# Optimization experiments

Measured on AMD Instinct MI355X. Metric: run time of the kernel, lower is better.

## Reference

```python
import jax, jax.numpy as jnp
import numpy as np

N_NODES = 50000
N_EDGES = 800000

def _sage_conv(x, src, dst, W, b, n_nodes):
    # DGL SAGEConv aggregator_type='gcn':
    #   h_neigh = (sum_{u in N(v)} x_u + x_v) / (in_deg(v) + 1)
    #   out = h_neigh @ W.T + b   (fc_self unused for gcn aggregator)
    agg = jax.ops.segment_sum(x[src], dst, num_segments=n_nodes)  # [N, d]
    deg = jax.ops.segment_sum(jnp.ones((src.shape[0],), x.dtype), dst, num_segments=n_nodes)
    h = (agg + x) / (deg + 1.0)[:, None]
    return h @ W.T + b

def setup_inputs() -> dict:
    key = jax.random.key(0)
    ks = jax.random.split(key, 9)
    d_in, d_hid, d_out = 128, 128, 64
    x = jax.random.normal(ks[0], (N_NODES, d_in), dtype=jnp.float32)
    src = jax.random.randint(ks[1], (N_EDGES,), 0, N_NODES, dtype=jnp.int32)
    dst = jax.random.randint(ks[2], (N_EDGES,), 0, N_NODES, dtype=jnp.int32)
    def glorot(k, shape):
        fan = shape[0] + shape[1]
        return jax.random.normal(k, shape, dtype=jnp.float32) * jnp.sqrt(2.0 / fan)
    W1 = glorot(ks[3], (d_hid, d_in))
    b1 = jnp.zeros((d_hid,), jnp.float32)
    W2 = glorot(ks[4], (d_hid, d_hid))
    b2 = jnp.zeros((d_hid,), jnp.float32)
    W3 = glorot(ks[5], (d_out, d_hid))
    b3 = jnp.zeros((d_out,), jnp.float32)
    return {"x": x, "src": src, "dst": dst, "W1": W1, "b1": b1,
            "W2": W2, "b2": b2, "W3": W3, "b3": b3}

def reference(x, src, dst, W1, b1, W2, b2, W3, b3):
    n = x.shape[0]
    h = jax.nn.relu(_sage_conv(x, src, dst, W1, b1, n))
    h = jax.nn.relu(_sage_conv(h, src, dst, W2, b2, n))
    h = jax.nn.sigmoid(_sage_conv(h, src, dst, W3, b3, n))
    return h
```

## Files before the change

kernel.cpp:

```cpp
#include <hip/hip_runtime.h>
#include <hip/hip_bf16.h>
#include <math.h>


#define NFEAT 128
#define BSH   6
#define NBUKP 1024
#define EPB2  1024
#define CAP   1600

typedef __attribute__((ext_vector_type(8))) short bf16x8;
typedef __attribute__((ext_vector_type(4))) float f32x4;

__device__ __forceinline__ unsigned short f2bf(float f) {
    unsigned u = __float_as_uint(f);
    u += 0x7fffu + ((u >> 16) & 1u);
    return (unsigned short)(u >> 16);
}
__device__ __forceinline__ float bflo(unsigned u) { return __uint_as_float(u << 16); }
__device__ __forceinline__ float bfhi(unsigned u) { return __uint_as_float(u & 0xffff0000u); }


__global__ __launch_bounds__(256) void cvt_scatter_kernel(
        const int* __restrict__ src, const int* __restrict__ dst,
        int* __restrict__ cursor, unsigned long long* __restrict__ pairs,
        int E, int SBLK,
        const float* __restrict__ x,  const float* __restrict__ W1,
        const float* __restrict__ W2, const float* __restrict__ W3,
        ushort* __restrict__ xb, ushort* __restrict__ w1,
        ushort* __restrict__ w2, ushort* __restrict__ w3,
        int nx, int n1, int n2, int n3) {
    __shared__ int hist[NBUKP];
    __shared__ int sc[NBUKP];
    __shared__ int lcur[NBUKP];
    __shared__ int lbase[NBUKP];
    __shared__ unsigned long long stage[EPB2];
    __shared__ int destIdx[EPB2];
    __shared__ int nLocalSh;

    const int t = threadIdx.x;

    if (blockIdx.x >= SBLK) {
        int i = (blockIdx.x - SBLK) * 256 + t;
        const float* s; ushort* d; int off;
        if (i < nx)                      { s = x;  d = xb; off = i; }
        else if (i < nx + n1)            { s = W1; d = w1; off = i - nx; }
        else if (i < nx + n1 + n2)       { s = W2; d = w2; off = i - nx - n1; }
        else if (i < nx + n1 + n2 + n3)  { s = W3; d = w3; off = i - nx - n1 - n2; }
        else return;
        float4 f = *(const float4*)(s + (size_t)off * 4);
        *(ushort4*)(d + (size_t)off * 4) = make_ushort4(f2bf(f.x), f2bf(f.y), f2bf(f.z), f2bf(f.w));
        return;
    }

#pragma unroll
    for (int k = 0; k < NBUKP / 256; ++k) {
        hist[t + 256 * k] = 0;
        lcur[t + 256 * k] = 0;
    }
    __syncthreads();

    const int base = blockIdx.x * EPB2;
    int bb[EPB2 / 256];
    unsigned long long pr[EPB2 / 256];
#pragma unroll
    for (int j = 0; j < EPB2 / 256; ++j) {
        int e = base + t + 256 * j;
        bb[j] = -1;
        if (e < E) {
            int s = src[e], d = dst[e];
            int b = d >> BSH;
            bb[j] = b;
            pr[j] = ((unsigned long long)(unsigned)d << 32) | (unsigned)s;
            atomicAdd(&hist[b], 1);
        }
    }
    __syncthreads();
#pragma unroll
    for (int k = 0; k < NBUKP / 256; ++k) sc[t + 256 * k] = hist[t + 256 * k];
    __syncthreads();
    for (int off = 1; off < NBUKP; off <<= 1) {
        int v0 = (t >= off) ? sc[t - off] : 0;
        int v1 = (t + 256 >= off) ? sc[t + 256 - off] : 0;
        int v2 = (t + 512 >= off) ? sc[t + 512 - off] : 0;
        int v3 = (t + 768 >= off) ? sc[t + 768 - off] : 0;
        __syncthreads();
        sc[t] += v0; sc[t + 256] += v1; sc[t + 512] += v2; sc[t + 768] += v3;
        __syncthreads();
    }
    if (t == 255) nLocalSh = sc[NBUKP - 1];
#pragma unroll
    for (int k = 0; k < NBUKP / 256; ++k) sc[t + 256 * k] -= hist[t + 256 * k];
    for (int b = t; b < NBUKP; b += 256) {
        int h = hist[b];
        if (h > 0) lbase[b] = atomicAdd(&cursor[b], h);
    }
    __syncthreads();
#pragma unroll
    for (int j = 0; j < EPB2 / 256; ++j) {
        int b = bb[j];
        if (b >= 0) {
            int slot = atomicAdd(&lcur[b], 1);
            int spos = sc[b] + slot;
            stage[spos] = pr[j];
            int rel = lbase[b] + slot;
            destIdx[spos] = (rel < CAP) ? (b * CAP + rel) : -1;
        }
    }
    __syncthreads();
    const int nLocal = nLocalSh;
#pragma unroll
    for (int j = 0; j < EPB2 / 256; ++j) {
        int i = t + 256 * j;
        if (i < nLocal && destIdx[i] >= 0) pairs[destIdx[i]] = stage[i];
    }
}


__global__ __launch_bounds__(512) void build_csr(const unsigned long long* __restrict__ pairs,
                                                 const int* __restrict__ cursor,
                                                 int* __restrict__ row_beg,
                                                 int* __restrict__ row_end,
                                                 float* __restrict__ deg_inv,
                                                 int* __restrict__ col_idx, int N) {
    __shared__ unsigned long long pairsL[CAP];
    __shared__ int srcS[CAP];
    __shared__ int nhist[64];
    __shared__ int npref[64];
    __shared__ int ncur[64];

    const int t = threadIdx.x;
    const int b = blockIdx.x;
    const int nodeBase = b << BSH;
    const int eBeg = b * CAP;
    int eCnt = cursor[b];
    if (eCnt > CAP) eCnt = CAP;

    if (t < 64) { nhist[t] = 0; ncur[t] = 0; }
    __syncthreads();

    for (int i = t; i < eCnt; i += 512) {
        unsigned long long p = pairs[eBeg + i];
        pairsL[i] = p;
        atomicAdd(&nhist[(int)(p >> 32) - nodeBase], 1);
    }
    __syncthreads();
    if (t < 64) npref[t] = nhist[t];
    __syncthreads();
    for (int off = 1; off < 64; off <<= 1) {
        int v = (t < 64 && t >= off) ? npref[t - off] : 0;
        __syncthreads();
        if (t < 64) npref[t] += v;
        __syncthreads();
    }
    if (t < 64) npref[t] -= nhist[t];
    if (t < 64 && nodeBase + t < N) {
        row_beg[nodeBase + t] = eBeg + npref[t];
        row_end[nodeBase + t] = eBeg + npref[t] + nhist[t];
        deg_inv[nodeBase + t] = 1.0f / (float)(nhist[t] + 1);
    }
    __syncthreads();
    for (int i = t; i < eCnt; i += 512) {
        unsigned long long p = pairsL[i];
        int d = (int)(p >> 32) - nodeBase;
        int slot = atomicAdd(&ncur[d], 1);
        srcS[npref[d] + slot] = (int)(unsigned)p;
    }
    __syncthreads();
    for (int i = t; i < eCnt; i += 512) col_idx[eBeg + i] = srcS[i];
}


#define ACC8(u)                                                     \
    a0 += bflo((u).x); a1 += bfhi((u).x);                           \
    a2 += bflo((u).y); a3 += bfhi((u).y);                           \
    a4 += bflo((u).z); a5 += bfhi((u).z);                           \
    a6 += bflo((u).w); a7 += bfhi((u).w);

template<int SECOND>
__global__ __launch_bounds__(256) void fused_agg_gemm_kernel(
        const ushort* __restrict__ Xb,
        const int* __restrict__ row_beg,
        const int* __restrict__ row_end,
        const float* __restrict__ deg_inv,
        const ushort* __restrict__ Wb,
        const float* __restrict__ bias,
        const ushort* __restrict__ W3b,
        const int* __restrict__ col_idx,
        ushort* __restrict__ outB, int N) {
    __shared__ ushort A[16][136];
    __shared__ ushort H2[SECOND ? 16 : 1][136];

    const int t    = threadIdx.x;
    const int w    = t >> 6;
    const int lane = t & 63;
    const int g    = lane >> 4;
    const int f    = lane & 15;
    const int base = blockIdx.x * 16;
    const uint4* X4 = (const uint4*)Xb;

    {
        const int v = base + w * 4 + g;
        const int beg = (v < N) ? row_beg[v] : 0;
        const int end = (v < N) ? row_end[v] : 0;
        const int deg = end - beg;

        uint4 us = (v < N) ? X4[(size_t)v * 16 + f] : make_uint4(0, 0, 0, 0);
        float inv = (v < N) ? deg_inv[v] : 0.f;

        int c0 = 0, c1 = 0;
        if (f < deg)      c0 = col_idx[beg + f];
        if (f + 16 < deg) c1 = col_idx[beg + 16 + f];

        float a0 = 0.f, a1 = 0.f, a2 = 0.f, a3 = 0.f;
        float a4 = 0.f, a5 = 0.f, a6 = 0.f, a7 = 0.f;

        const int nf = deg < 32 ? deg : 32;
        int j = 0;
        for (; j + 7 < nf; j += 8) {
            const int cc = (j & 16) ? c1 : c0;
            int s0 = __shfl(cc, (j & 15) + 0, 16);
            int s1 = __shfl(cc, (j & 15) + 1, 16);
            int s2 = __shfl(cc, (j & 15) + 2, 16);
            int s3 = __shfl(cc, (j & 15) + 3, 16);
            int s4 = __shfl(cc, (j & 15) + 4, 16);
            int s5 = __shfl(cc, (j & 15) + 5, 16);
            int s6 = __shfl(cc, (j & 15) + 6, 16);
            int s7 = __shfl(cc, (j & 15) + 7, 16);
            uint4 u0 = X4[(size_t)s0 * 16 + f];
            uint4 u1 = X4[(size_t)s1 * 16 + f];
            uint4 u2 = X4[(size_t)s2 * 16 + f];
            uint4 u3 = X4[(size_t)s3 * 16 + f];
            uint4 u4 = X4[(size_t)s4 * 16 + f];
            uint4 u5 = X4[(size_t)s5 * 16 + f];
            uint4 u6 = X4[(size_t)s6 * 16 + f];
            uint4 u7 = X4[(size_t)s7 * 16 + f];
            ACC8(u0); ACC8(u1); ACC8(u2); ACC8(u3);
            ACC8(u4); ACC8(u5); ACC8(u6); ACC8(u7);
        }
        for (; j < nf; ++j) {
            const int cc = (j & 16) ? c1 : c0;
            int s0 = __shfl(cc, j & 15, 16);
            uint4 u = X4[(size_t)s0 * 16 + f];
            ACC8(u);
        }
        for (int e = beg + 32; e < end; ++e) {
            uint4 u = X4[(size_t)col_idx[e] * 16 + f];
            ACC8(u);
        }

        if (v < N) {
            uint4 r;
            r.x = (unsigned)f2bf((a0 + bflo(us.x)) * inv) | ((unsigned)f2bf((a1 + bfhi(us.x)) * inv) << 16);
            r.y = (unsigned)f2bf((a2 + bflo(us.y)) * inv) | ((unsigned)f2bf((a3 + bfhi(us.y)) * inv) << 16);
            r.z = (unsigned)f2bf((a4 + bflo(us.z)) * inv) | ((unsigned)f2bf((a5 + bfhi(us.z)) * inv) << 16);
            r.w = (unsigned)f2bf((a6 + bflo(us.w)) * inv) | ((unsigned)f2bf((a7 + bfhi(us.w)) * inv) << 16);
            ((uint4*)&A[w * 4 + g][0])[f] = r;
        }
    }
    __syncthreads();

    const int m    = lane & 15;
    const int quad = lane >> 4;
    f32x4 acc0 = {0.f, 0.f, 0.f, 0.f};
    f32x4 acc1 = {0.f, 0.f, 0.f, 0.f};
    {
        const ushort* arow = &A[m][quad * 8];
        const ushort* wrow = Wb + (size_t)(w * 32 + m) * NFEAT + quad * 8;
#pragma unroll
        for (int k0 = 0; k0 < NFEAT; k0 += 32) {
            bf16x8 a  = *(const bf16x8*)(arow + k0);
            bf16x8 bA = *(const bf16x8*)(wrow + k0);
            bf16x8 bB = *(const bf16x8*)(wrow + 16 * NFEAT + k0);
            acc0 = __builtin_amdgcn_mfma_f32_16x16x32_bf16(a, bA, acc0, 0, 0, 0);
            acc1 = __builtin_amdgcn_mfma_f32_16x16x32_bf16(a, bB, acc1, 0, 0, 0);
        }
    }
    const float bv0 = bias[w * 32 + m];
    const float bv1 = bias[w * 32 + 16 + m];

    if (!SECOND) {
#pragma unroll
        for (int r = 0; r < 4; ++r) {
            int row = base + quad * 4 + r;
            if (row < N) {
                outB[(size_t)row * NFEAT + w * 32 + m]      = f2bf(fmaxf(acc0[r] + bv0, 0.f));
                outB[(size_t)row * NFEAT + w * 32 + 16 + m] = f2bf(fmaxf(acc1[r] + bv1, 0.f));
            }
        }
    } else {
#pragma unroll
        for (int r = 0; r < 4; ++r) {
            H2[quad * 4 + r][w * 32 + m]      = f2bf(fmaxf(acc0[r] + bv0, 0.f));
            H2[quad * 4 + r][w * 32 + 16 + m] = f2bf(fmaxf(acc1[r] + bv1, 0.f));
        }
        __syncthreads();
        f32x4 acc3 = {0.f, 0.f, 0.f, 0.f};
        const ushort* hrow  = &H2[m][quad * 8];
        const ushort* w3row = W3b + (size_t)(w * 16 + m) * NFEAT + quad * 8;
#pragma unroll
        for (int k0 = 0; k0 < NFEAT; k0 += 32) {
            bf16x8 a = *(const bf16x8*)(hrow + k0);
            bf16x8 b = *(const bf16x8*)(w3row + k0);
            acc3 = __builtin_amdgcn_mfma_f32_16x16x32_bf16(a, b, acc3, 0, 0, 0);
        }
#pragma unroll
        for (int r = 0; r < 4; ++r) {
            int row = base + quad * 4 + r;
            if (row < N) outB[(size_t)row * 64 + w * 16 + m] = f2bf(acc3[r]);
        }
    }
}


__global__ __launch_bounds__(256) void agg64_sigmoid_kernel(const ushort* __restrict__ Gb,
                                                            const int* __restrict__ row_beg,
                                                            const int* __restrict__ row_end,
                                                            const float* __restrict__ deg_inv,
                                                            const int* __restrict__ col_idx,
                                                            const float* __restrict__ bias,
                                                            float* __restrict__ out, int N) {
    const int wp   = blockIdx.x * (blockDim.x >> 6) + (threadIdx.x >> 6);
    const int lane = threadIdx.x & 63;
    const int half = lane >> 5;
    const int hl   = lane & 31;
    const int v    = wp * 2 + half;
    const bool act = (v < N);

    int beg = 0, end = 0;
    if (act) { beg = row_beg[v]; end = row_end[v]; }
    const int deg = end - beg;
    const unsigned* Gu = (const unsigned*)Gb;

    int cidx = 0;
    if (hl < deg) cidx = col_idx[beg + hl];

    float a0 = 0.f, a1 = 0.f, b0 = 0.f, b1 = 0.f;
    float c0 = 0.f, c1 = 0.f, d0 = 0.f, d1 = 0.f;
    const int nfast = deg < 32 ? deg : 32;
    int j = 0;
    for (; j + 7 < nfast; j += 8) {
        int s0 = __shfl(cidx, j + 0, 32);
        int s1 = __shfl(cidx, j + 1, 32);
        int s2 = __shfl(cidx, j + 2, 32);
        int s3 = __shfl(cidx, j + 3, 32);
        int s4 = __shfl(cidx, j + 4, 32);
        int s5 = __shfl(cidx, j + 5, 32);
        int s6 = __shfl(cidx, j + 6, 32);
        int s7 = __shfl(cidx, j + 7, 32);
        unsigned u0 = Gu[(size_t)s0 * 32 + hl];
        unsigned u1 = Gu[(size_t)s1 * 32 + hl];
        unsigned u2 = Gu[(size_t)s2 * 32 + hl];
        unsigned u3 = Gu[(size_t)s3 * 32 + hl];
        unsigned u4 = Gu[(size_t)s4 * 32 + hl];
        unsigned u5 = Gu[(size_t)s5 * 32 + hl];
        unsigned u6 = Gu[(size_t)s6 * 32 + hl];
        unsigned u7 = Gu[(size_t)s7 * 32 + hl];
        a0 += bflo(u0); a1 += bfhi(u0);
        b0 += bflo(u1); b1 += bfhi(u1);
        c0 += bflo(u2); c1 += bfhi(u2);
        d0 += bflo(u3); d1 += bfhi(u3);
        a0 += bflo(u4); a1 += bfhi(u4);
        b0 += bflo(u5); b1 += bfhi(u5);
        c0 += bflo(u6); c1 += bfhi(u6);
        d0 += bflo(u7); d1 += bfhi(u7);
    }
    for (; j + 3 < nfast; j += 4) {
        int s0 = __shfl(cidx, j + 0, 32);
        int s1 = __shfl(cidx, j + 1, 32);
        int s2 = __shfl(cidx, j + 2, 32);
        int s3 = __shfl(cidx, j + 3, 32);
        unsigned u0 = Gu[(size_t)s0 * 32 + hl];
        unsigned u1 = Gu[(size_t)s1 * 32 + hl];
        unsigned u2 = Gu[(size_t)s2 * 32 + hl];
        unsigned u3 = Gu[(size_t)s3 * 32 + hl];
        a0 += bflo(u0); a1 += bfhi(u0);
        b0 += bflo(u1); b1 += bfhi(u1);
        c0 += bflo(u2); c1 += bfhi(u2);
        d0 += bflo(u3); d1 += bfhi(u3);
    }
    for (; j < nfast; ++j) {
        int s0 = __shfl(cidx, j, 32);
        unsigned u0 = Gu[(size_t)s0 * 32 + hl];
        a0 += bflo(u0); a1 += bfhi(u0);
    }
    for (int e = beg + 32; e < end; ++e) {
        unsigned u0 = Gu[(size_t)col_idx[e] * 32 + hl];
        a0 += bflo(u0); a1 += bfhi(u0);
    }
    if (act) {
        unsigned us = Gu[(size_t)v * 32 + hl];
        float inv = deg_inv[v];
        float r0 = (a0 + b0 + c0 + d0 + bflo(us)) * inv + bias[hl * 2 + 0];
        float r1 = (a1 + b1 + c1 + d1 + bfhi(us)) * inv + bias[hl * 2 + 1];
        r0 = 1.0f / (1.0f + __expf(-r0));
        r1 = 1.0f / (1.0f + __expf(-r1));
        *(float2*)(out + (size_t)v * 64 + hl * 2) = make_float2(r0, r1);
    }
}


static inline size_t align256(size_t x) { return (x + 255) & ~(size_t)255; }

extern "C" void kernel_launch(void* const* d_in, const int* in_sizes, int n_in,
                              void* d_out, int out_size, void* d_ws, size_t ws_size,
                              hipStream_t stream) {
    const float* x   = (const float*)d_in[0];
    const int*   src = (const int*)d_in[1];
    const int*   dst = (const int*)d_in[2];
    const float* W1  = (const float*)d_in[3];
    const float* b1  = (const float*)d_in[4];
    const float* W2  = (const float*)d_in[5];
    const float* b2  = (const float*)d_in[6];
    const float* W3  = (const float*)d_in[7];
    const float* b3  = (const float*)d_in[8];
    float*       out = (float*)d_out;

    const int N = in_sizes[0] / NFEAT;
    const int E = in_sizes[1];
    const int D_OUT = in_sizes[7] / NFEAT;
    const int NBUK = (N + (1 << BSH) - 1) >> BSH;
    const int SBLK = (E + EPB2 - 1) / EPB2;

    char* ws = (char*)d_ws;
    int* row_beg      = (int*)ws;  ws += align256((size_t)N * 4);
    int* row_end      = (int*)ws;  ws += align256((size_t)N * 4);
    float* deg_inv    = (float*)ws; ws += align256((size_t)N * 4);
    int* cursor       = (int*)ws;  ws += align256((size_t)NBUKP * 4);
    int* col_idx      = (int*)ws;  ws += align256((size_t)NBUK * CAP * 4);
    ushort* w1bf      = (ushort*)ws; ws += align256((size_t)NFEAT * NFEAT * 2);
    ushort* w2bf      = (ushort*)ws; ws += align256((size_t)NFEAT * NFEAT * 2);
    ushort* w3bf      = (ushort*)ws; ws += align256((size_t)D_OUT * NFEAT * 2);
    ushort* xbf       = (ushort*)ws; ws += align256((size_t)N * NFEAT * 2);
    ushort* h1bf      = (ushort*)ws; ws += align256((size_t)N * NFEAT * 2);
    ushort* gbf = xbf;
    unsigned long long* pairs = (unsigned long long*)h1bf;

    const int nx = N * NFEAT / 4;
    const int n1 = NFEAT * NFEAT / 4, n2 = NFEAT * NFEAT / 4, n3 = D_OUT * NFEAT / 4;
    const int CVTB = (nx + n1 + n2 + n3 + 255) / 256;

    hipMemsetAsync(cursor, 0, (size_t)NBUKP * 4, stream);
    cvt_scatter_kernel<<<SBLK + CVTB, 256, 0, stream>>>(
        src, dst, cursor, pairs, E, SBLK,
        x, W1, W2, W3, xbf, w1bf, w2bf, w3bf, nx, n1, n2, n3);

    build_csr<<<NBUK, 512, 0, stream>>>(pairs, cursor, row_beg, row_end, deg_inv, col_idx, N);

    const int fusedBlocks = (N + 15) / 16;
    const int agg64Blocks = (N + 7) / 8;

    fused_agg_gemm_kernel<0><<<fusedBlocks, 256, 0, stream>>>(
        xbf, row_beg, row_end, deg_inv, w1bf, b1, nullptr, col_idx, h1bf, N);
    fused_agg_gemm_kernel<1><<<fusedBlocks, 256, 0, stream>>>(
        h1bf, row_beg, row_end, deg_inv, w2bf, b2, w3bf, col_idx, gbf, N);
    agg64_sigmoid_kernel<<<agg64Blocks, 256, 0, stream>>>(
        gbf, row_beg, row_end, deg_inv, col_idx, b3, out, N);
}
```

Measured before the change: 233.4 us.

## Merge all stages into one cooperative persistent kernel with grid syncs

Replaces the memset plus five separate kernel launches with a single cooperative kernel that runs the convert, scatter, CSR build, two fused aggregate-GEMM layers and the final aggregation as phases separated by grid-wide barriers. Blocks loop over virtual block indices, and shared memory is a single reused byte buffer. The aim is to remove launch overhead and inter-kernel gaps. In exchange, occupancy is capped at the cooperative grid size, the convert phase no longer overlaps the scatter phase, build_csr drops from 512 to 256 threads, and every phase boundary adds a grid sync.

```diff
diff --git a/kernel.cpp b/kernel.cpp
--- a/kernel.cpp
+++ b/kernel.cpp
@@ -1,6 +1,9 @@
 #include <hip/hip_runtime.h>
+#include <hip/hip_cooperative_groups.h>
 #include <hip/hip_bf16.h>
 #include <math.h>
+
+namespace cg = cooperative_groups;
 
 
 #define NFEAT 128
@@ -8,9 +11,23 @@
 #define NBUKP 1024
 #define EPB2  1024
 #define CAP   1600
-
+#define SMEM_BYTES 28680
+
+typedef unsigned long long ull;
 typedef __attribute__((ext_vector_type(8))) short bf16x8;
 typedef __attribute__((ext_vector_type(4))) float f32x4;
+
+struct MegaArgs {
+    const int* src; const int* dst;
+    int* cursor; ull* pairs;
+    const float* x; const float* W1; const float* W2; const float* W3;
+    const float* b1; const float* b2; const float* b3;
+    ushort* xb; ushort* w1b; ushort* w2b; ushort* w3b;
+    int* row_beg; int* row_end; float* deg_inv; int* col_idx;
+    ushort* h1; ushort* g; float* out;
+    int E, N, SBLK, NBUK, fusedB, agg64B;
+    int nx, n1, n2, n3, cvt_total;
+};
 
 __device__ __forceinline__ unsigned short f2bf(float f) {
     unsigned u = __float_as_uint(f);
@@ -21,57 +38,45 @@
 __device__ __forceinline__ float bfhi(unsigned u) { return __uint_as_float(u & 0xffff0000u); }
 
 
-__global__ __launch_bounds__(256) void cvt_scatter_kernel(
-        const int* __restrict__ src, const int* __restrict__ dst,
-        int* __restrict__ cursor, unsigned long long* __restrict__ pairs,
-        int E, int SBLK,
-        const float* __restrict__ x,  const float* __restrict__ W1,
-        const float* __restrict__ W2, const float* __restrict__ W3,
-        ushort* __restrict__ xb, ushort* __restrict__ w1,
-        ushort* __restrict__ w2, ushort* __restrict__ w3,
-        int nx, int n1, int n2, int n3) {
-    __shared__ int hist[NBUKP];
-    __shared__ int sc[NBUKP];
-    __shared__ int lcur[NBUKP];
-    __shared__ int lbase[NBUKP];
-    __shared__ unsigned long long stage[EPB2];
-    __shared__ int destIdx[EPB2];
-    __shared__ int nLocalSh;
-
-    const int t = threadIdx.x;
-
-    if (blockIdx.x >= SBLK) {
-        int i = (blockIdx.x - SBLK) * 256 + t;
+__device__ void phase_cvt(const MegaArgs& a, int gtid, int gsz) {
+    for (int i = gtid; i < a.cvt_total; i += gsz) {
         const float* s; ushort* d; int off;
-        if (i < nx)                      { s = x;  d = xb; off = i; }
-        else if (i < nx + n1)            { s = W1; d = w1; off = i - nx; }
-        else if (i < nx + n1 + n2)       { s = W2; d = w2; off = i - nx - n1; }
-        else if (i < nx + n1 + n2 + n3)  { s = W3; d = w3; off = i - nx - n1 - n2; }
-        else return;
+        if (i < a.nx)                              { s = a.x;  d = a.xb;  off = i; }
+        else if (i < a.nx + a.n1)                  { s = a.W1; d = a.w1b; off = i - a.nx; }
+        else if (i < a.nx + a.n1 + a.n2)           { s = a.W2; d = a.w2b; off = i - a.nx - a.n1; }
+        else                                       { s = a.W3; d = a.w3b; off = i - a.nx - a.n1 - a.n2; }
         float4 f = *(const float4*)(s + (size_t)off * 4);
         *(ushort4*)(d + (size_t)off * 4) = make_ushort4(f2bf(f.x), f2bf(f.y), f2bf(f.z), f2bf(f.w));
-        return;
-    }
-
-#pragma unroll
-    for (int k = 0; k < NBUKP / 256; ++k) {
-        hist[t + 256 * k] = 0;
-        lcur[t + 256 * k] = 0;
-    }
-    __syncthreads();
-
-    const int base = blockIdx.x * EPB2;
+    }
+    for (int i = gtid; i < NBUKP; i += gsz) a.cursor[i] = 0;
+}
+
+
+__device__ void phase_scatter(const MegaArgs& a, int vb, int t, char* smem) {
+    ull* stage    = (ull*)smem;
+    int* hist     = (int*)(smem + 8192);
+    int* sc       = (int*)(smem + 12288);
+    int* lcur     = (int*)(smem + 16384);
+    int* lbase    = (int*)(smem + 20480);
+    int* destIdx  = (int*)(smem + 24576);
+    int* nLocalSh = (int*)(smem + 28672);
+
+#pragma unroll
+    for (int k = 0; k < NBUKP / 256; ++k) { hist[t + 256 * k] = 0; lcur[t + 256 * k] = 0; }
+    __syncthreads();
+
+    const int base = vb * EPB2;
     int bb[EPB2 / 256];
-    unsigned long long pr[EPB2 / 256];
+    ull pr[EPB2 / 256];
 #pragma unroll
     for (int j = 0; j < EPB2 / 256; ++j) {
         int e = base + t + 256 * j;
         bb[j] = -1;
-        if (e < E) {
-            int s = src[e], d = dst[e];
+        if (e < a.E) {
+            int s = a.src[e], d = a.dst[e];
             int b = d >> BSH;
             bb[j] = b;
-            pr[j] = ((unsigned long long)(unsigned)d << 32) | (unsigned)s;
+            pr[j] = ((ull)(unsigned)d << 32) | (unsigned)s;
             atomicAdd(&hist[b], 1);
         }
     }
@@ -88,12 +93,12 @@
         sc[t] += v0; sc[t + 256] += v1; sc[t + 512] += v2; sc[t + 768] += v3;
         __syncthreads();
     }
-    if (t == 255) nLocalSh = sc[NBUKP - 1];
+    if (t == 255) *nLocalSh = sc[NBUKP - 1];
 #pragma unroll
     for (int k = 0; k < NBUKP / 256; ++k) sc[t + 256 * k] -= hist[t + 256 * k];
     for (int b = t; b < NBUKP; b += 256) {
         int h = hist[b];
-        if (h > 0) lbase[b] = atomicAdd(&cursor[b], h);
+        if (h > 0) lbase[b] = atomicAdd(&a.cursor[b], h);
     }
     __syncthreads();
 #pragma unroll
@@ -108,39 +113,33 @@
         }
     }
     __syncthreads();
-    const int nLocal = nLocalSh;
+    const int nLocal = *nLocalSh;
 #pragma unroll
     for (int j = 0; j < EPB2 / 256; ++j) {
         int i = t + 256 * j;
-        if (i < nLocal && destIdx[i] >= 0) pairs[destIdx[i]] = stage[i];
-    }
-}
-
-
-__global__ __launch_bounds__(512) void build_csr(const unsigned long long* __restrict__ pairs,
-                                                 const int* __restrict__ cursor,
-                                                 int* __restrict__ row_beg,
-                                                 int* __restrict__ row_end,
-                                                 float* __restrict__ deg_inv,
-                                                 int* __restrict__ col_idx, int N) {
-    __shared__ unsigned long long pairsL[CAP];
-    __shared__ int srcS[CAP];
-    __shared__ int nhist[64];
-    __shared__ int npref[64];
-    __shared__ int ncur[64];
-
-    const int t = threadIdx.x;
-    const int b = blockIdx.x;
-    const int nodeBase = b << BSH;
-    const int eBeg = b * CAP;
-    int eCnt = cursor[b];
+        if (i < nLocal && destIdx[i] >= 0) a.pairs[destIdx[i]] = stage[i];
+    }
+    __syncthreads();
+}
+
+
+__device__ void phase_csr(const MegaArgs& a, int vb, int t, char* smem) {
+    ull* pairsL = (ull*)smem;
+    int* srcS   = (int*)(smem + 12800);
+    int* nhist  = (int*)(smem + 19200);
+    int* npref  = (int*)(smem + 19456);
+    int* ncur   = (int*)(smem + 19712);
+
+    const int nodeBase = vb << BSH;
+    const int eBeg = vb * CAP;
+    int eCnt = a.cursor[vb];
     if (eCnt > CAP) eCnt = CAP;
 
     if (t < 64) { nhist[t] = 0; ncur[t] = 0; }
     __syncthreads();
 
-    for (int i = t; i < eCnt; i += 512) {
-        unsigned long long p = pairs[eBeg + i];
+    for (int i = t; i < eCnt; i += 256) {
+        ull p = a.pairs[eBeg + i];
         pairsL[i] = p;
         atomicAdd(&nhist[(int)(p >> 32) - nodeBase], 1);
     }
@@ -154,20 +153,21 @@
         __syncthreads();
     }
     if (t < 64) npref[t] -= nhist[t];
-    if (t < 64 && nodeBase + t < N) {
-        row_beg[nodeBase + t] = eBeg + npref[t];
-        row_end[nodeBase + t] = eBeg + npref[t] + nhist[t];
-        deg_inv[nodeBase + t] = 1.0f / (float)(nhist[t] + 1);
-    }
-    __syncthreads();
-    for (int i = t; i < eCnt; i += 512) {
-        unsigned long long p = pairsL[i];
+    if (t < 64 && nodeBase + t < a.N) {
+        a.row_beg[nodeBase + t] = eBeg + npref[t];
+        a.row_end[nodeBase + t] = eBeg + npref[t] + nhist[t];
+        a.deg_inv[nodeBase + t] = 1.0f / (float)(nhist[t] + 1);
+    }
+    __syncthreads();
+    for (int i = t; i < eCnt; i += 256) {
+        ull p = pairsL[i];
         int d = (int)(p >> 32) - nodeBase;
         int slot = atomicAdd(&ncur[d], 1);
         srcS[npref[d] + slot] = (int)(unsigned)p;
     }
     __syncthreads();
-    for (int i = t; i < eCnt; i += 512) col_idx[eBeg + i] = srcS[i];
+    for (int i = t; i < eCnt; i += 256) a.col_idx[eBeg + i] = srcS[i];
+    __syncthreads();
 }
 
 
@@ -178,35 +178,33 @@
     a6 += bflo((u).w); a7 += bfhi((u).w);
 
 template<int SECOND>
-__global__ __launch_bounds__(256) void fused_agg_gemm_kernel(
-        const ushort* __restrict__ Xb,
-        const int* __restrict__ row_beg,
-        const int* __restrict__ row_end,
-        const float* __restrict__ deg_inv,
-        const ushort* __restrict__ Wb,
-        const float* __restrict__ bias,
-        const ushort* __restrict__ W3b,
-        const int* __restrict__ col_idx,
-        ushort* __restrict__ outB, int N) {
-    __shared__ ushort A[16][136];
-    __shared__ ushort H2[SECOND ? 16 : 1][136];
-
-    const int t    = threadIdx.x;
+__device__ void phase_fused(const MegaArgs& a_, int vb, int t, char* smem) {
+    ushort (*A)[136]  = (ushort(*)[136])smem;
+    ushort (*H2)[136] = (ushort(*)[136])(smem + 4352);
+
+    const ushort* Xb   = SECOND ? a_.h1  : a_.xb;
+    const ushort* Wb   = SECOND ? a_.w2b : a_.w1b;
+    const float*  bias = SECOND ? a_.b2  : a_.b1;
+    const ushort* W3b  = a_.w3b;
+    ushort*       outB = SECOND ? a_.g   : a_.h1;
+    const int N = a_.N;
+    const int* __restrict__ col_idx = a_.col_idx;
+
     const int w    = t >> 6;
     const int lane = t & 63;
     const int g    = lane >> 4;
     const int f    = lane & 15;
-    const int base = blockIdx.x * 16;
+    const int base = vb * 16;
     const uint4* X4 = (const uint4*)Xb;
 
     {
         const int v = base + w * 4 + g;
-        const int beg = (v < N) ? row_beg[v] : 0;
-        const int end = (v < N) ? row_end[v] : 0;
+        const int beg = (v < N) ? a_.row_beg[v] : 0;
+        const int end = (v < N) ? a_.row_end[v] : 0;
         const int deg = end - beg;
 
         uint4 us = (v < N) ? X4[(size_t)v * 16 + f] : make_uint4(0, 0, 0, 0);
-        float inv = (v < N) ? deg_inv[v] : 0.f;
+        float inv = (v < N) ? a_.deg_inv[v] : 0.f;
 
         int c0 = 0, c1 = 0;
         if (f < deg)      c0 = col_idx[beg + f];
@@ -269,11 +267,11 @@
         const ushort* wrow = Wb + (size_t)(w * 32 + m) * NFEAT + quad * 8;
 #pragma unroll
         for (int k0 = 0; k0 < NFEAT; k0 += 32) {
-            bf16x8 a  = *(const bf16x8*)(arow + k0);
+            bf16x8 av = *(const bf16x8*)(arow + k0);
             bf16x8 bA = *(const bf16x8*)(wrow + k0);
             bf16x8 bB = *(const bf16x8*)(wrow + 16 * NFEAT + k0);
-            acc0 = __builtin_amdgcn_mfma_f32_16x16x32_bf16(a, bA, acc0, 0, 0, 0);
-            acc1 = __builtin_amdgcn_mfma_f32_16x16x32_bf16(a, bB, acc1, 0, 0, 0);
+            acc0 = __builtin_amdgcn_mfma_f32_16x16x32_bf16(av, bA, acc0, 0, 0, 0);
+            acc1 = __builtin_amdgcn_mfma_f32_16x16x32_bf16(av, bB, acc1, 0, 0, 0);
         }
     }
     const float bv0 = bias[w * 32 + m];
@@ -300,9 +298,9 @@
         const ushort* w3row = W3b + (size_t)(w * 16 + m) * NFEAT + quad * 8;
 #pragma unroll
         for (int k0 = 0; k0 < NFEAT; k0 += 32) {
-            bf16x8 a = *(const bf16x8*)(hrow + k0);
-            bf16x8 b = *(const bf16x8*)(w3row + k0);
-            acc3 = __builtin_amdgcn_mfma_f32_16x16x32_bf16(a, b, acc3, 0, 0, 0);
+            bf16x8 av = *(const bf16x8*)(hrow + k0);
+            bf16x8 bv = *(const bf16x8*)(w3row + k0);
+            acc3 = __builtin_amdgcn_mfma_f32_16x16x32_bf16(av, bv, acc3, 0, 0, 0);
         }
 #pragma unroll
         for (int r = 0; r < 4; ++r) {
@@ -310,30 +308,25 @@
             if (row < N) outB[(size_t)row * 64 + w * 16 + m] = f2bf(acc3[r]);
         }
     }
-}
-
-
-__global__ __launch_bounds__(256) void agg64_sigmoid_kernel(const ushort* __restrict__ Gb,
-                                                            const int* __restrict__ row_beg,
-                                                            const int* __restrict__ row_end,
-                                                            const float* __restrict__ deg_inv,
-                                                            const int* __restrict__ col_idx,
-                                                            const float* __restrict__ bias,
-                                                            float* __restrict__ out, int N) {
-    const int wp   = blockIdx.x * (blockDim.x >> 6) + (threadIdx.x >> 6);
-    const int lane = threadIdx.x & 63;
+    __syncthreads();
+}
+
+
+__device__ void phase_agg64(const MegaArgs& a, int vb, int t) {
+    const int wp   = vb * 4 + (t >> 6);
+    const int lane = t & 63;
     const int half = lane >> 5;
     const int hl   = lane & 31;
     const int v    = wp * 2 + half;
-    const bool act = (v < N);
+    const bool act = (v < a.N);
 
     int beg = 0, end = 0;
-    if (act) { beg = row_beg[v]; end = row_end[v]; }
+    if (act) { beg = a.row_beg[v]; end = a.row_end[v]; }
     const int deg = end - beg;
-    const unsigned* Gu = (const unsigned*)Gb;
+    const unsigned* Gu = (const unsigned*)a.g;
 
     int cidx = 0;
-    if (hl < deg) cidx = col_idx[beg + hl];
+    if (hl < deg) cidx = a.col_idx[beg + hl];
 
     float a0 = 0.f, a1 = 0.f, b0 = 0.f, b1 = 0.f;
     float c0 = 0.f, c1 = 0.f, d0 = 0.f, d1 = 0.f;
@@ -385,18 +378,63 @@
         a0 += bflo(u0); a1 += bfhi(u0);
     }
     for (int e = beg + 32; e < end; ++e) {
-        unsigned u0 = Gu[(size_t)col_idx[e] * 32 + hl];
+        unsigned u0 = Gu[(size_t)a.col_idx[e] * 32 + hl];
         a0 += bflo(u0); a1 += bfhi(u0);
     }
     if (act) {
         unsigned us = Gu[(size_t)v * 32 + hl];
-        float inv = deg_inv[v];
-        float r0 = (a0 + b0 + c0 + d0 + bflo(us)) * inv + bias[hl * 2 + 0];
-        float r1 = (a1 + b1 + c1 + d1 + bfhi(us)) * inv + bias[hl * 2 + 1];
+        float inv = a.deg_inv[v];
+        float r0 = (a0 + b0 + c0 + d0 + bflo(us)) * inv + a.b3[hl * 2 + 0];
+        float r1 = (a1 + b1 + c1 + d1 + bfhi(us)) * inv + a.b3[hl * 2 + 1];
         r0 = 1.0f / (1.0f + __expf(-r0));
         r1 = 1.0f / (1.0f + __expf(-r1));
-        *(float2*)(out + (size_t)v * 64 + hl * 2) = make_float2(r0, r1);
-    }
+        *(float2*)(a.out + (size_t)v * 64 + hl * 2) = make_float2(r0, r1);
+    }
+}
+
+
+__global__ __launch_bounds__(256) void mega_kernel(MegaArgs a) {
+    __shared__ __align__(16) char smem[SMEM_BYTES];
+    cg::grid_group grid = cg::this_grid();
+    const int t = threadIdx.x;
+    const int gtid = blockIdx.x * 256 + t;
+    const int gsz  = gridDim.x * 256;
+
+    phase_cvt(a, gtid, gsz);
+    __threadfence(); grid.sync();
+    for (int vb = blockIdx.x; vb < a.SBLK; vb += gridDim.x) phase_scatter(a, vb, t, smem);
+    __threadfence(); grid.sync();
+    for (int vb = blockIdx.x; vb < a.NBUK; vb += gridDim.x) phase_csr(a, vb, t, smem);
+    __threadfence(); grid.sync();
+    for (int vb = blockIdx.x; vb < a.fusedB; vb += gridDim.x) phase_fused<0>(a, vb, t, smem);
+    __threadfence(); grid.sync();
+    for (int vb = blockIdx.x; vb < a.fusedB; vb += gridDim.x) phase_fused<1>(a, vb, t, smem);
+    __threadfence(); grid.sync();
+    for (int vb = blockIdx.x; vb < a.agg64B; vb += gridDim.x) phase_agg64(a, vb, t);
+}
+
+
+__global__ __launch_bounds__(256) void k_cvt(MegaArgs a) {
+    phase_cvt(a, blockIdx.x * 256 + threadIdx.x, gridDim.x * 256);
+}
+__global__ __launch_bounds__(256) void k_scatter(MegaArgs a) {
+    __shared__ __align__(16) char smem[SMEM_BYTES];
+    for (int vb = blockIdx.x; vb < a.SBLK; vb += gridDim.x) phase_scatter(a, vb, threadIdx.x, smem);
+}
+__global__ __launch_bounds__(256) void k_csr(MegaArgs a) {
+    __shared__ __align__(16) char smem[SMEM_BYTES];
+    for (int vb = blockIdx.x; vb < a.NBUK; vb += gridDim.x) phase_csr(a, vb, threadIdx.x, smem);
+}
+__global__ __launch_bounds__(256) void k_fused0(MegaArgs a) {
+    __shared__ __align__(16) char smem[SMEM_BYTES];
+    for (int vb = blockIdx.x; vb < a.fusedB; vb += gridDim.x) phase_fused<0>(a, vb, threadIdx.x, smem);
+}
+__global__ __launch_bounds__(256) void k_fused1(MegaArgs a) {
+    __shared__ __align__(16) char smem[SMEM_BYTES];
+    for (int vb = blockIdx.x; vb < a.fusedB; vb += gridDim.x) phase_fused<1>(a, vb, threadIdx.x, smem);
+}
+__global__ __launch_bounds__(256) void k_agg64(MegaArgs a) {
+    for (int vb = blockIdx.x; vb < a.agg64B; vb += gridDim.x) phase_agg64(a, vb, threadIdx.x);
 }
 
 
@@ -434,26 +472,47 @@
     ushort* xbf       = (ushort*)ws; ws += align256((size_t)N * NFEAT * 2);
     ushort* h1bf      = (ushort*)ws; ws += align256((size_t)N * NFEAT * 2);
     ushort* gbf = xbf;
-    unsigned long long* pairs = (unsigned long long*)h1bf;
-
-    const int nx = N * NFEAT / 4;
-    const int n1 = NFEAT * NFEAT / 4, n2 = NFEAT * NFEAT / 4, n3 = D_OUT * NFEAT / 4;
-    const int CVTB = (nx + n1 + n2 + n3 + 255) / 256;
-
-    hipMemsetAsync(cursor, 0, (size_t)NBUKP * 4, stream);
-    cvt_scatter_kernel<<<SBLK + CVTB, 256, 0, stream>>>(
-        src, dst, cursor, pairs, E, SBLK,
-        x, W1, W2, W3, xbf, w1bf, w2bf, w3bf, nx, n1, n2, n3);
-
-    build_csr<<<NBUK, 512, 0, stream>>>(pairs, cursor, row_beg, row_end, deg_inv, col_idx, N);
-
-    const int fusedBlocks = (N + 15) / 16;
-    const int agg64Blocks = (N + 7) / 8;
-
-    fused_agg_gemm_kernel<0><<<fusedBlocks, 256, 0, stream>>>(
-        xbf, row_beg, row_end, deg_inv, w1bf, b1, nullptr, col_idx, h1bf, N);
-    fused_agg_gemm_kernel<1><<<fusedBlocks, 256, 0, stream>>>(
-        h1bf, row_beg, row_end, deg_inv, w2bf, b2, w3bf, col_idx, gbf, N);
-    agg64_sigmoid_kernel<<<agg64Blocks, 256, 0, stream>>>(
-        gbf, row_beg, row_end, deg_inv, col_idx, b3, out, N);
-}
+    ull* pairs = (ull*)h1bf;
+
+    MegaArgs ma;
+    ma.src = src; ma.dst = dst;
+    ma.cursor = cursor; ma.pairs = pairs;
+    ma.x = x; ma.W1 = W1; ma.W2 = W2; ma.W3 = W3;
+    ma.b1 = b1; ma.b2 = b2; ma.b3 = b3;
+    ma.xb = xbf; ma.w1b = w1bf; ma.w2b = w2bf; ma.w3b = w3bf;
+    ma.row_beg = row_beg; ma.row_end = row_end; ma.deg_inv = deg_inv; ma.col_idx = col_idx;
+    ma.h1 = h1bf; ma.g = gbf; ma.out = out;
+    ma.E = E; ma.N = N; ma.SBLK = SBLK; ma.NBUK = NBUK;
+    ma.fusedB = (N + 15) / 16;
+    ma.agg64B = (N + 7) / 8;
+    ma.nx = N * NFEAT / 4;
+    ma.n1 = NFEAT * NFEAT / 4; ma.n2 = NFEAT * NFEAT / 4; ma.n3 = D_OUT * NFEAT / 4;
+    ma.cvt_total = ma.nx + ma.n1 + ma.n2 + ma.n3;
+
+    static int g_nB = 0;
+    if (g_nB == 0) {
+        int bpc = 0;
+        if (hipOccupancyMaxActiveBlocksPerMultiprocessor(&bpc, (const void*)mega_kernel, 256, 0) != hipSuccess || bpc < 1)
+            bpc = 1;
+        int dev = 0; hipGetDevice(&dev);
+        hipDeviceProp_t prop;
+        int cus = 256;
+        if (hipGetDeviceProperties(&prop, dev) == hipSuccess && prop.multiProcessorCount > 0)
+            cus = prop.multiProcessorCount;
+        g_nB = bpc * cus;
+        if (g_nB < 64) g_nB = 64;
+    }
+
+    void* kargs[] = { (void*)&ma };
+    hipError_t err = hipLaunchCooperativeKernel((const void*)mega_kernel,
+                                                dim3(g_nB), dim3(256), kargs, 0, stream);
+    if (err != hipSuccess) {
+        (void)hipGetLastError();
+        k_cvt<<<(ma.cvt_total + 255) / 256, 256, 0, stream>>>(ma);
+        k_scatter<<<SBLK, 256, 0, stream>>>(ma);
+        k_csr<<<NBUK, 256, 0, stream>>>(ma);
+        k_fused0<<<ma.fusedB, 256, 0, stream>>>(ma);
+        k_fused1<<<ma.fusedB, 256, 0, stream>>>(ma);
+        k_agg64<<<ma.agg64B, 256, 0, stream>>>(ma);
+    }
+}
```

Result: slower. 656.8 us (+181.4%).
